# Optimization experiments

Hardware: AMD Instinct MI355X
Metric: run time of the kernel (lower is better)

The kernel has to match this reference:

```python
import jax, jax.numpy as jnp
import numpy as np

SMALL = -1000.0

def _crf_loss(pred, transitions, tags, seq_len):
    B, T, L = pred.shape
    START, STOP = L - 2, L - 1
    # pred[:, :, -2] = pred[:, :, -1] = small
    pred = pred.at[:, :, START].set(SMALL).at[:, :, STOP].set(SMALL)
    # start / end padding states
    start_state = jnp.full((B, 1, L), SMALL, pred.dtype).at[:, :, START].set(0.0)
    end_state = jnp.zeros((B, 1, L), pred.dtype)
    padded = jnp.concatenate([start_state, pred, end_state], axis=1)  # [B, T+2, L]
    b_idx = jnp.arange(B)
    padded = padded.at[b_idx, seq_len + 1, :].set(SMALL)
    padded = padded.at[b_idx, seq_len + 1, STOP].set(0.0)
    padded_t = jnp.transpose(padded, (1, 0, 2))  # [T+2, B, L]

    def step(prev, emit):
        # prev: [B, L] (from-label), emit: [B, L] (to-label)
        new = jax.nn.logsumexp(prev[:, :, None] + transitions[None, :, :] + emit[:, None, :], axis=1)
        return new, new

    _, alphas = jax.lax.scan(step, padded_t[0], padded_t[1:])  # [T+1, B, L]
    gathered = alphas[seq_len, b_idx, :]  # [B, L] (alphas at position seq_len)
    pred_paths_scores = jnp.sum(jax.nn.logsumexp(gathered, axis=1))

    # real path emission score
    pos = jnp.arange(T)
    mask = (pos[None, :] < seq_len[:, None]).astype(pred.dtype)  # [B, T]
    emit_score = jnp.take_along_axis(pred, tags[:, :, None], axis=2)[:, :, 0]  # [B, T]
    real_path_score = jnp.sum(emit_score * mask)

    # real path transition score
    start_tag = jnp.full((B, 1), START, tags.dtype)
    end_tag = jnp.zeros((B, 1), tags.dtype)
    padded_tags = jnp.concatenate([start_tag, tags, end_tag], axis=1)  # [B, T+2]
    padded_tags = padded_tags.at[b_idx, seq_len + 1].set(STOP)
    trans_score = transitions[padded_tags[:, :-1], padded_tags[:, 1:]]  # [B, T+1]
    tpos = jnp.arange(T + 1)
    tmask = (tpos[None, :] < (seq_len + 1)[:, None]).astype(pred.dtype)
    real_path_score = real_path_score + jnp.sum(trans_score * tmask)

    return pred_paths_scores - real_path_score


def setup_inputs() -> dict:
    key = jax.random.key(0)
    k1, k2, k3, k4 = jax.random.split(key, 4)
    B, T, L = 128, 1024, 128
    pred = jax.random.normal(k1, (B, T, L), dtype=jnp.float32)
    transitions = jax.random.normal(k2, (L, L), dtype=jnp.float32) * 0.1
    tags = jax.random.randint(k3, (B, T), 0, L - 2)  # real labels only, [0, L-3]
    seq_len = jax.random.randint(k4, (B,), 1, T + 1)
    return {"pred": pred, "transitions": transitions, "tags": tags, "seq_len": seq_len}


def reference(pred, transitions, tags, seq_len):
    return _crf_loss(pred, transitions, tags, seq_len)
```

## Files before the change

kernel.cpp:

```cpp
#include <hip/hip_runtime.h>

constexpr int L      = 128;
constexpr int TDIM   = 1024;
constexpr int NBATCH = 128;
constexpr int START  = L - 2;
constexpr int STOP   = L - 1;
constexpr int BSUB   = 16;
constexpr int NBLK   = NBATCH / BSUB;

typedef short bf16x8 __attribute__((ext_vector_type(8)));
typedef float f32x4  __attribute__((ext_vector_type(4)));
typedef int   i32x4  __attribute__((ext_vector_type(4)));

union B4 { i32x4 i; bf16x8 v; };

__device__ __forceinline__ short f2bf(float f) {
    unsigned x = __float_as_uint(f);
    return (short)((x + 0x7fffu + ((x >> 16) & 1u)) >> 16);
}
__device__ __forceinline__ unsigned pkbf(float lo, float hi) {
    unsigned r;
    asm("v_cvt_pk_bf16_f32 %0, %1, %2" : "=v"(r) : "v"(lo), "v"(hi));
    return r;
}

__global__ __launch_bounds__(256)
void crf_pexp(const float* __restrict__ pred, const int* __restrict__ seq_len,
              unsigned short* __restrict__ pexp)
{
    int gid  = blockIdx.x * 256 + threadIdx.x;
    int lane = gid & 63;
    int c    = (gid >> 6) & 3;
    int row  = (gid >> 8) & 1023;
    int blk  = gid >> 18;
    int l15 = lane & 15, l4 = lane >> 4;
    int b = blk * 16 + l15;
    bool live = row < seq_len[b];

    const float* src = pred + ((size_t)b * TDIM + row) * L + 32 * c + 4 * l4;
    f32x4 v0 = *(const f32x4*)(src);
    f32x4 v1 = *(const f32x4*)(src + 16);

    float e0[4], e1[4];
#pragma unroll
    for (int r = 0; r < 4; ++r) {
        int s0 = 32 * c + 4 * l4 + r;
        int s1 = s0 + 16;
        e0[r] = (live && s0 < 126) ? __expf(v0[r]) : 0.0f;
        e1[r] = (live && s1 < 126) ? __expf(v1[r]) : 0.0f;
    }
    i32x4 out;
    out[0] = (int)pkbf(e0[0], e0[1]);
    out[1] = (int)pkbf(e0[2], e0[3]);
    out[2] = (int)pkbf(e1[0], e1[1]);
    out[3] = (int)pkbf(e1[2], e1[3]);
    *(i32x4*)((char*)pexp + (size_t)gid * 16) = out;
}

struct PB { i32x4 c[4]; };
struct PF { f32x4 q[8]; };

template<bool PEXP>
__global__ __launch_bounds__(64, 1)
void crf_chain(const float* __restrict__ pred,
               const float* __restrict__ trans,
               const int* __restrict__ seq_len,
               const unsigned short* __restrict__ pexp,
               float* __restrict__ fwd_out)
{
    const int lane = threadIdx.x;
    const int l15 = lane & 15, l4 = lane >> 4;
    const int blk = blockIdx.x;
    const int b   = blk * BSUB + l15;

    bf16x8 A[8][4];
#pragma unroll
    for (int T = 0; T < 8; ++T)
#pragma unroll
        for (int kt = 0; kt < 4; ++kt) {
            bf16x8 v;
#pragma unroll
            for (int e = 0; e < 8; ++e) {
                int s = 16 * kt + 64 * (e >> 2) + 4 * l4 + (e & 3);
                v[e] = f2bf(__expf(trans[s * L + 16 * T + l15]));
            }
            A[T][kt] = v;
        }

    const int srow1 = seq_len[b] + 1;

    int mx = srow1;
#pragma unroll
    for (int d = 1; d < 16; d <<= 1) mx = max(mx, __shfl_xor(mx, d));
    const int tmaxR = __builtin_amdgcn_readfirstlane((mx + 3) & ~3);

    B4 B[4];
#pragma unroll
    for (int kt = 0; kt < 4; ++kt) B[kt].i = (i32x4){0, 0, 0, 0};
    if (l4 == 3) B[3].i[3] = 0x3F80;

    float C = 0.0f;

    const char* pxb = (const char*)pexp + (size_t)blk * 1024 * 4096;
    const float* pfb = pred + (size_t)b * TDIM * L + 4 * l4;

    auto loadPB = [&](PB& p, int row) {
        const i32x4* s = (const i32x4*)(pxb + (size_t)row * 4096) + lane;
        p.c[0] = s[0]; p.c[1] = s[64]; p.c[2] = s[128]; p.c[3] = s[192];
    };
    auto loadPF = [&](PF& p, int row) {
        const f32x4* s = (const f32x4*)(pfb + (size_t)row * L);
#pragma unroll
        for (int T = 0; T < 8; ++T) p.q[T] = s[T * 4];
    };

    auto stepP = [&](int t, PB& pb) {
        f32x4 acc[8];
#pragma unroll
        for (int T = 0; T < 8; ++T) acc[T] = (f32x4){0.f, 0.f, 0.f, 0.f};
#pragma unroll
        for (int kt = 0; kt < 4; ++kt)
#pragma unroll
            for (int T = 0; T < 8; ++T)
                acc[T] = __builtin_amdgcn_mfma_f32_16x16x32_bf16(A[T][kt], B[kt].v, acc[T], 0, 0, 0);

        if (l4 == 3 && t == srow1)
            fwd_out[b] = __logf(acc[7][3]) + C;

        float u[8][4];
#pragma unroll
        for (int T = 0; T < 8; ++T) {
            int c = T >> 1, h = (T & 1) * 2;
            unsigned w0 = (unsigned)pb.c[c][h + 0];
            unsigned w1 = (unsigned)pb.c[c][h + 1];
            u[T][0] = acc[T][0] * __uint_as_float(w0 << 16);
            u[T][1] = acc[T][1] * __uint_as_float(w0 & 0xffff0000u);
            u[T][2] = acc[T][2] * __uint_as_float(w1 << 16);
            u[T][3] = acc[T][3] * __uint_as_float(w1 & 0xffff0000u);
        }
        loadPB(pb, min(t + 3, TDIM - 1));

        float m[8];
#pragma unroll
        for (int T = 0; T < 8; ++T)
            m[T] = fmaxf(fmaxf(u[T][0], u[T][1]), fmaxf(u[T][2], u[T][3]));
        float mx4 = fmaxf(fmaxf(fmaxf(m[0], m[1]), fmaxf(m[2], m[3])),
                          fmaxf(fmaxf(m[4], m[5]), fmaxf(m[6], m[7])));
        if (__ballot(mx4 > 0x1p80f)) {
#pragma unroll
            for (int T = 0; T < 8; ++T)
#pragma unroll
                for (int r = 0; r < 4; ++r) u[T][r] *= 0x1p-64f;
            C += 44.3614195558365f;
        }

#pragma unroll
        for (int kt = 0; kt < 4; ++kt) {
            B[kt].i[0] = (int)pkbf(u[kt][0], u[kt][1]);
            B[kt].i[1] = (int)pkbf(u[kt][2], u[kt][3]);
            B[kt].i[2] = (int)pkbf(u[kt + 4][0], u[kt + 4][1]);
            B[kt].i[3] = (int)pkbf(u[kt + 4][2], u[kt + 4][3]);
        }
    };

    auto stepF = [&](int t, PF& pf) {
        f32x4 acc[8];
#pragma unroll
        for (int T = 0; T < 8; ++T) acc[T] = (f32x4){0.f, 0.f, 0.f, 0.f};
#pragma unroll
        for (int kt = 0; kt < 4; ++kt)
#pragma unroll
            for (int T = 0; T < 8; ++T)
                acc[T] = __builtin_amdgcn_mfma_f32_16x16x32_bf16(A[T][kt], B[kt].v, acc[T], 0, 0, 0);

        if (l4 == 3 && t == srow1)
            fwd_out[b] = __logf(acc[7][3]) + C;

        const bool live = (t < srow1);
        float u[8][4];
#pragma unroll
        for (int T = 0; T < 8; ++T)
#pragma unroll
            for (int r = 0; r < 4; ++r) {
                bool dead = !live || (T == 7 && l4 == 3 && r >= 2);
                u[T][r] = dead ? 0.0f : acc[T][r] * __expf(pf.q[T][r]);
            }
        loadPF(pf, min(t + 1, TDIM - 1));

        float m[8];
#pragma unroll
        for (int T = 0; T < 8; ++T)
            m[T] = fmaxf(fmaxf(u[T][0], u[T][1]), fmaxf(u[T][2], u[T][3]));
        float mx4 = fmaxf(fmaxf(fmaxf(m[0], m[1]), fmaxf(m[2], m[3])),
                          fmaxf(fmaxf(m[4], m[5]), fmaxf(m[6], m[7])));
        if (__ballot(mx4 > 0x1p80f)) {
#pragma unroll
            for (int T = 0; T < 8; ++T)
#pragma unroll
                for (int r = 0; r < 4; ++r) u[T][r] *= 0x1p-64f;
            C += 44.3614195558365f;
        }
#pragma unroll
        for (int kt = 0; kt < 4; ++kt) {
            B[kt].i[0] = (int)pkbf(u[kt][0], u[kt][1]);
            B[kt].i[1] = (int)pkbf(u[kt][2], u[kt][3]);
            B[kt].i[2] = (int)pkbf(u[kt + 4][0], u[kt + 4][1]);
            B[kt].i[3] = (int)pkbf(u[kt + 4][2], u[kt + 4][3]);
        }
    };

    if constexpr (PEXP) {
        PB pa, pb_, pc, pd;
        loadPB(pa, 0); loadPB(pb_, min(1, TDIM - 1));
        loadPB(pc, min(2, TDIM - 1)); loadPB(pd, min(3, TDIM - 1));
        for (int t0 = 0; t0 < tmaxR; t0 += 4) {
            stepP(t0 + 1, pa);
            stepP(t0 + 2, pb_);
            stepP(t0 + 3, pc);
            stepP(t0 + 4, pd);
        }
    } else {
        PF fa, fb;
        loadPF(fa, 0); loadPF(fb, min(1, TDIM - 1));
        for (int t0 = 0; t0 < tmaxR; t0 += 2) {
            stepF(t0 + 1, fa);
            stepF(t0 + 2, fb);
        }
    }
}

__global__ __launch_bounds__(256)
void crf_score(const float* __restrict__ pred,
               const float* __restrict__ trans,
               const int* __restrict__ tags,
               const int* __restrict__ seq_len,
               float* __restrict__ score_out)
{
    const int b = blockIdx.x;
    const int tid = threadIdx.x;
    const int sl = seq_len[b];
    const int* tg = tags + b * TDIM;

    float s = 0.0f;
    for (int t = tid; t < sl; t += 256) {
        int tag = tg[t];
        s += pred[((long)b * TDIM + t) * L + tag];
        int prev = (t == 0) ? START : tg[t - 1];
        s += trans[prev * L + tag];
    }
    if (tid == 0) s += trans[tg[sl - 1] * L + STOP];

    __shared__ float red[4];
#pragma unroll
    for (int d = 1; d < 64; d <<= 1) s += __shfl_xor(s, d);
    if ((tid & 63) == 0) red[tid >> 6] = s;
    __syncthreads();
    if (tid == 0) score_out[b] = (red[0] + red[1]) + (red[2] + red[3]);
}

__global__ __launch_bounds__(128)
void crf_combine(const float* __restrict__ fwd,
                 const float* __restrict__ real,
                 float* __restrict__ out)
{
    const int tid = threadIdx.x;
    float s = fwd[tid] - real[tid];
#pragma unroll
    for (int d = 1; d < 64; d <<= 1) s += __shfl_xor(s, d);
    __shared__ float red[2];
    if ((tid & 63) == 0) red[tid >> 6] = s;
    __syncthreads();
    if (tid == 0) out[0] = red[0] + red[1];
}

extern "C" void kernel_launch(void* const* d_in, const int* in_sizes, int n_in,
                              void* d_out, int out_size, void* d_ws, size_t ws_size,
                              hipStream_t stream)
{
    const float* pred    = (const float*)d_in[0];
    const float* trans   = (const float*)d_in[1];
    const int*   tags    = (const int*)d_in[2];
    const int*   seq_len = (const int*)d_in[3];

    float* ws   = (float*)d_ws;
    float* fwd  = ws;
    float* real = ws + 128;

    const size_t pexp_bytes = (size_t)NBLK * 1024 * 4096;
    if (ws_size >= 1024 + pexp_bytes) {
        unsigned short* pexp = (unsigned short*)((char*)d_ws + 1024);
        crf_pexp<<<8192, 256, 0, stream>>>(pred, seq_len, pexp);
        crf_chain<true><<<NBLK, 64, 0, stream>>>(pred, trans, seq_len, pexp, fwd);
    } else {
        crf_chain<false><<<NBLK, 64, 0, stream>>>(pred, trans, seq_len, nullptr, fwd);
    }
    crf_score  <<<NBATCH, 256, 0, stream>>>(pred, trans, tags, seq_len, real);
    crf_combine<<<1, 128, 0, stream>>>(fwd, real, (float*)d_out);
}
```

Baseline: 538.3 us.

## Pack chain waves into one block, defer rescale check, drop per-step result store

Launches the forward recurrence as one 512-thread block with eight waves on a single CU, replacing eight separate 64-thread blocks. The overflow rescale check now runs every other step and is applied one step late, which takes the max-reduction and ballot off the critical path of half the steps. The final log-sum result is kept in registers and written once after the loop instead of by a conditional store inside each step. Prefetch depth drops from four rows to two, and the first MFMA of each chain now uses a zero accumulator. Eight waves sharing one CU contend for its MFMA units and memory bandwidth, and delaying the rescale lets values grow one extra step before scaling.

Measured after the change: 722.6 us. +34.2%, slower.

```diff
diff --git a/kernel.cpp b/kernel.cpp
--- a/kernel.cpp
+++ b/kernel.cpp
@@ -6,7 +6,7 @@
 constexpr int START  = L - 2;
 constexpr int STOP   = L - 1;
 constexpr int BSUB   = 16;
-constexpr int NBLK   = NBATCH / BSUB;
+constexpr int NWAVE  = NBATCH / BSUB;
 
 typedef short bf16x8 __attribute__((ext_vector_type(8)));
 typedef float f32x4  __attribute__((ext_vector_type(4)));
@@ -61,17 +61,18 @@
 struct PF { f32x4 q[8]; };
 
 template<bool PEXP>
-__global__ __launch_bounds__(64, 1)
+__global__ __launch_bounds__(512, 1)
 void crf_chain(const float* __restrict__ pred,
                const float* __restrict__ trans,
                const int* __restrict__ seq_len,
                const unsigned short* __restrict__ pexp,
                float* __restrict__ fwd_out)
 {
-    const int lane = threadIdx.x;
+    const int tid  = threadIdx.x;
+    const int lane = tid & 63;
+    const int wave = tid >> 6;
     const int l15 = lane & 15, l4 = lane >> 4;
-    const int blk = blockIdx.x;
-    const int b   = blk * BSUB + l15;
+    const int b   = wave * BSUB + l15;
 
     bf16x8 A[8][4];
 #pragma unroll
@@ -92,16 +93,20 @@
     int mx = srow1;
 #pragma unroll
     for (int d = 1; d < 16; d <<= 1) mx = max(mx, __shfl_xor(mx, d));
-    const int tmaxR = __builtin_amdgcn_readfirstlane((mx + 3) & ~3);
+    const int tmaxR = __builtin_amdgcn_readfirstlane((mx + 1) & ~1);
 
     B4 B[4];
 #pragma unroll
     for (int kt = 0; kt < 4; ++kt) B[kt].i = (i32x4){0, 0, 0, 0};
     if (l4 == 3) B[3].i[3] = 0x3F80;
 
+    const f32x4 Z4 = {0.f, 0.f, 0.f, 0.f};
+
     float C = 0.0f;
-
-    const char* pxb = (const char*)pexp + (size_t)blk * 1024 * 4096;
+    bool  applyScale = false;
+    float res = 1.0f, resC = 0.0f;
+
+    const char*  pxb = (const char*)pexp + (size_t)wave * 1024 * 4096;
     const float* pfb = pred + (size_t)b * TDIM * L + 4 * l4;
 
     auto loadPB = [&](PB& p, int row) {
@@ -114,44 +119,48 @@
         for (int T = 0; T < 8; ++T) p.q[T] = s[T * 4];
     };
 
-    auto stepP = [&](int t, PB& pb) {
+    auto stepP = [&](int t, PB& pb, bool chk) {
         f32x4 acc[8];
 #pragma unroll
-        for (int T = 0; T < 8; ++T) acc[T] = (f32x4){0.f, 0.f, 0.f, 0.f};
-#pragma unroll
-        for (int kt = 0; kt < 4; ++kt)
+        for (int T = 0; T < 8; ++T)
+            acc[T] = __builtin_amdgcn_mfma_f32_16x16x32_bf16(A[T][0], B[0].v, Z4, 0, 0, 0);
+#pragma unroll
+        for (int kt = 1; kt < 4; ++kt)
 #pragma unroll
             for (int T = 0; T < 8; ++T)
                 acc[T] = __builtin_amdgcn_mfma_f32_16x16x32_bf16(A[T][kt], B[kt].v, acc[T], 0, 0, 0);
 
-        if (l4 == 3 && t == srow1)
-            fwd_out[b] = __logf(acc[7][3]) + C;
+        bool hit = (t == srow1);
+        res  = hit ? acc[7][3] : res;
+        resC = hit ? C : resC;
 
         float u[8][4];
 #pragma unroll
         for (int T = 0; T < 8; ++T) {
-            int c = T >> 1, h = (T & 1) * 2;
-            unsigned w0 = (unsigned)pb.c[c][h + 0];
-            unsigned w1 = (unsigned)pb.c[c][h + 1];
+            int cI = T >> 1, h = (T & 1) * 2;
+            unsigned w0 = (unsigned)pb.c[cI][h + 0];
+            unsigned w1 = (unsigned)pb.c[cI][h + 1];
             u[T][0] = acc[T][0] * __uint_as_float(w0 << 16);
             u[T][1] = acc[T][1] * __uint_as_float(w0 & 0xffff0000u);
             u[T][2] = acc[T][2] * __uint_as_float(w1 << 16);
             u[T][3] = acc[T][3] * __uint_as_float(w1 & 0xffff0000u);
         }
-        loadPB(pb, min(t + 3, TDIM - 1));
-
-        float m[8];
-#pragma unroll
-        for (int T = 0; T < 8; ++T)
-            m[T] = fmaxf(fmaxf(u[T][0], u[T][1]), fmaxf(u[T][2], u[T][3]));
-        float mx4 = fmaxf(fmaxf(fmaxf(m[0], m[1]), fmaxf(m[2], m[3])),
-                          fmaxf(fmaxf(m[4], m[5]), fmaxf(m[6], m[7])));
-        if (__ballot(mx4 > 0x1p80f)) {
+        if (applyScale) {
 #pragma unroll
             for (int T = 0; T < 8; ++T)
 #pragma unroll
                 for (int r = 0; r < 4; ++r) u[T][r] *= 0x1p-64f;
             C += 44.3614195558365f;
+        }
+        applyScale = false;
+        if (chk) {
+            float m[8];
+#pragma unroll
+            for (int T = 0; T < 8; ++T)
+                m[T] = fmaxf(fmaxf(u[T][0], u[T][1]), fmaxf(u[T][2], u[T][3]));
+            float mx4 = fmaxf(fmaxf(fmaxf(m[0], m[1]), fmaxf(m[2], m[3])),
+                              fmaxf(fmaxf(m[4], m[5]), fmaxf(m[6], m[7])));
+            applyScale = (__ballot(mx4 > 0x1p80f) != 0ull);
         }
 
 #pragma unroll
@@ -161,20 +170,23 @@
             B[kt].i[2] = (int)pkbf(u[kt + 4][0], u[kt + 4][1]);
             B[kt].i[3] = (int)pkbf(u[kt + 4][2], u[kt + 4][3]);
         }
+        loadPB(pb, min(t + 1, TDIM - 1));
     };
 
-    auto stepF = [&](int t, PF& pf) {
+    auto stepF = [&](int t, PF& pf, bool chk) {
         f32x4 acc[8];
 #pragma unroll
-        for (int T = 0; T < 8; ++T) acc[T] = (f32x4){0.f, 0.f, 0.f, 0.f};
-#pragma unroll
-        for (int kt = 0; kt < 4; ++kt)
+        for (int T = 0; T < 8; ++T)
+            acc[T] = __builtin_amdgcn_mfma_f32_16x16x32_bf16(A[T][0], B[0].v, Z4, 0, 0, 0);
+#pragma unroll
+        for (int kt = 1; kt < 4; ++kt)
 #pragma unroll
             for (int T = 0; T < 8; ++T)
                 acc[T] = __builtin_amdgcn_mfma_f32_16x16x32_bf16(A[T][kt], B[kt].v, acc[T], 0, 0, 0);
 
-        if (l4 == 3 && t == srow1)
-            fwd_out[b] = __logf(acc[7][3]) + C;
+        bool hit = (t == srow1);
+        res  = hit ? acc[7][3] : res;
+        resC = hit ? C : resC;
 
         const bool live = (t < srow1);
         float u[8][4];
@@ -185,20 +197,22 @@
                 bool dead = !live || (T == 7 && l4 == 3 && r >= 2);
                 u[T][r] = dead ? 0.0f : acc[T][r] * __expf(pf.q[T][r]);
             }
-        loadPF(pf, min(t + 1, TDIM - 1));
-
-        float m[8];
-#pragma unroll
-        for (int T = 0; T < 8; ++T)
-            m[T] = fmaxf(fmaxf(u[T][0], u[T][1]), fmaxf(u[T][2], u[T][3]));
-        float mx4 = fmaxf(fmaxf(fmaxf(m[0], m[1]), fmaxf(m[2], m[3])),
-                          fmaxf(fmaxf(m[4], m[5]), fmaxf(m[6], m[7])));
-        if (__ballot(mx4 > 0x1p80f)) {
+        if (applyScale) {
 #pragma unroll
             for (int T = 0; T < 8; ++T)
 #pragma unroll
                 for (int r = 0; r < 4; ++r) u[T][r] *= 0x1p-64f;
             C += 44.3614195558365f;
+        }
+        applyScale = false;
+        if (chk) {
+            float m[8];
+#pragma unroll
+            for (int T = 0; T < 8; ++T)
+                m[T] = fmaxf(fmaxf(u[T][0], u[T][1]), fmaxf(u[T][2], u[T][3]));
+            float mx4 = fmaxf(fmaxf(fmaxf(m[0], m[1]), fmaxf(m[2], m[3])),
+                              fmaxf(fmaxf(m[4], m[5]), fmaxf(m[6], m[7])));
+            applyScale = (__ballot(mx4 > 0x1p80f) != 0ull);
         }
 #pragma unroll
         for (int kt = 0; kt < 4; ++kt) {
@@ -207,26 +221,27 @@
             B[kt].i[2] = (int)pkbf(u[kt + 4][0], u[kt + 4][1]);
             B[kt].i[3] = (int)pkbf(u[kt + 4][2], u[kt + 4][3]);
         }
+        loadPF(pf, min(t + 1, TDIM - 1));
     };
 
     if constexpr (PEXP) {
-        PB pa, pb_, pc, pd;
-        loadPB(pa, 0); loadPB(pb_, min(1, TDIM - 1));
-        loadPB(pc, min(2, TDIM - 1)); loadPB(pd, min(3, TDIM - 1));
-        for (int t0 = 0; t0 < tmaxR; t0 += 4) {
-            stepP(t0 + 1, pa);
-            stepP(t0 + 2, pb_);
-            stepP(t0 + 3, pc);
-            stepP(t0 + 4, pd);
+        PB pa, pb_;
+        loadPB(pa, 0); loadPB(pb_, 1);
+        for (int t0 = 0; t0 < tmaxR; t0 += 2) {
+            stepP(t0 + 1, pa, true);
+            stepP(t0 + 2, pb_, false);
         }
     } else {
         PF fa, fb;
-        loadPF(fa, 0); loadPF(fb, min(1, TDIM - 1));
+        loadPF(fa, 0); loadPF(fb, 1);
         for (int t0 = 0; t0 < tmaxR; t0 += 2) {
-            stepF(t0 + 1, fa);
-            stepF(t0 + 2, fb);
+            stepF(t0 + 1, fa, true);
+            stepF(t0 + 2, fb, false);
         }
     }
+
+    if (l4 == 3)
+        fwd_out[b] = __logf(res) + resC;
 }
 
 __global__ __launch_bounds__(256)
@@ -286,13 +301,13 @@
     float* fwd  = ws;
     float* real = ws + 128;
 
-    const size_t pexp_bytes = (size_t)NBLK * 1024 * 4096;
+    const size_t pexp_bytes = (size_t)NWAVE * 1024 * 4096;
     if (ws_size >= 1024 + pexp_bytes) {
         unsigned short* pexp = (unsigned short*)((char*)d_ws + 1024);
         crf_pexp<<<8192, 256, 0, stream>>>(pred, seq_len, pexp);
-        crf_chain<true><<<NBLK, 64, 0, stream>>>(pred, trans, seq_len, pexp, fwd);
+        crf_chain<true><<<1, 512, 0, stream>>>(pred, trans, seq_len, pexp, fwd);
     } else {
-        crf_chain<false><<<NBLK, 64, 0, stream>>>(pred, trans, seq_len, nullptr, fwd);
+        crf_chain<false><<<1, 512, 0, stream>>>(pred, trans, seq_len, nullptr, fwd);
     }
     crf_score  <<<NBATCH, 256, 0, stream>>>(pred, trans, tags, seq_len, real);
     crf_combine<<<1, 128, 0, stream>>>(fwd, real, (float*)d_out);
```
